# Kernel tuning notes

Hardware: AMD Instinct MI355X
Metric: run time of the kernel (lower is better)

Reference implementation:

```python
import jax, jax.numpy as jnp
import numpy as np

TAU = 0.07
COS_EPS = 1e-8   # torch F.cosine_similarity eps
L1_EPS = 1e-12   # torch F.normalize eps
MM_EPS = 1e-8    # min-max renorm eps

B, C, H, W = 64, 256, 32, 32
S, D = 512, 256


def setup_inputs() -> dict:
    key = jax.random.key(0)
    k1, k2, k3, k4 = jax.random.split(key, 4)
    scale = 1.0 / np.sqrt(D)
    return {
        "image_patches": jax.random.normal(k1, (B, C, H, W), dtype=jnp.float32),
        "text_tokens": jax.random.normal(k2, (B, S, D), dtype=jnp.float32),
        "Wv": jax.random.normal(k3, (D, D), dtype=jnp.float32) * scale,
        "bv": jnp.zeros((D,), dtype=jnp.float32),
        "Wt": jax.random.normal(k4, (D, D), dtype=jnp.float32) * scale,
        "bt": jnp.zeros((D,), dtype=jnp.float32),
    }


def _linear(x, Wgt, b):
    return x @ Wgt.T + b


def _l2n(x, axis=-1):
    n = jnp.maximum(jnp.linalg.norm(x, axis=axis, keepdims=True), COS_EPS)
    return x / n


def _sym_ce_diag(sim):
    # sim [..., N, N]; mean of -log_softmax diagonals along both class axes
    lsm_r = jax.nn.log_softmax(sim, axis=-1)
    lsm_c = jax.nn.log_softmax(sim, axis=-2)
    d_r = jnp.diagonal(lsm_r, axis1=-2, axis2=-1)
    d_c = jnp.diagonal(lsm_c, axis1=-2, axis2=-1)
    return 0.5 * (-jnp.mean(d_r) - jnp.mean(d_c))


def reference(image_patches, text_tokens, Wv, bv, Wt, bt):
    b, c, h, w = image_patches.shape
    hw = h * w
    # b c h w -> b (h w) c, then adapters
    patches = image_patches.reshape(b, c, hw).transpose(0, 2, 1)  # [b, hw, c]
    patches = _linear(patches, Wv, bv)          # [b, hw, d]
    tokens = _linear(text_tokens, Wt, bt)       # [b, s, d]

    # global embeddings: mean-pool then adapter (adapter applied twice on vision path)
    g_img = _linear(jnp.mean(patches, axis=1), Wv, bv)  # [b, d]
    g_txt = _linear(jnp.mean(tokens, axis=1), Wt, bt)   # [b, d]

    # global contrastive loss (cosine sim / tau, symmetric CE over batch)
    g_sim = (_l2n(g_img) @ _l2n(g_txt).T) / TAU         # [b, b]
    global_loss = _sym_ce_diag(g_sim)

    # fine-grained alignment
    sim = jnp.einsum('bpd,bsd->bps', patches, tokens)   # [b, hw, s]
    mn = jnp.min(sim, axis=1, keepdims=True)
    mx = jnp.max(sim, axis=1, keepdims=True)
    sim = (sim - mn) / (mx - mn + MM_EPS)
    sigma = 1.0 / hw
    sim = jnp.where(sim < sigma, 0.0, sim)
    # L1 normalize over patch dim (torch F.normalize p=1 dim=1)
    weights = sim / jnp.maximum(jnp.sum(jnp.abs(sim), axis=1, keepdims=True), L1_EPS)
    lgve = jnp.einsum('bps,bpd->bsd', weights, patches)  # [b, s, d]

    # fine-grained contrastive loss: cosine sim between grouped-vision and text tokens
    f_sim = jnp.einsum('bid,bjd->bij', _l2n(lgve), _l2n(tokens)) / TAU  # [b, s, s]
    fine_loss = _sym_ce_diag(f_sim)

    return global_loss + fine_loss
```

## Files before the change

### kernel.cpp

```cpp
#include <hip/hip_runtime.h>
#include <math.h>

#define BB   64
#define HWP  1024
#define SS   512
#define DD   256
#define TAU_INV (1.0f/0.07f)
#define SIGMA   (1.0f/1024.0f)

typedef unsigned short us;
typedef __attribute__((ext_vector_type(8))) short short8v;
typedef __attribute__((ext_vector_type(8))) unsigned short ushort8v;
typedef __attribute__((ext_vector_type(4))) float floatx4;

__device__ __forceinline__ float bf2f(us u) {
    return __uint_as_float((unsigned)u << 16);
}
__device__ __forceinline__ us f2bf(float f) {
    unsigned u = __float_as_uint(f);
    u += 0x7FFFu + ((u >> 16) & 1u);
    return (us)(u >> 16);
}
__device__ __forceinline__ void split_bf(float v, us& h, us& l) {
    h = f2bf(v);
    l = f2bf(v - bf2f(h));
}

__global__ void zero_out_k(float* out) { if (threadIdx.x == 0) out[0] = 0.0f; }

enum { OPM_F32_ROW = 0, OPM_F32_COL = 1, OPM_SPL_ROW = 2, OPM_SPL_COL = 3,
       OPM_B16_COL = 4, OPM_B16_ROW = 5, OPM_WGT_COL = 6 };
enum { OUT_F32 = 0, OUT_B16 = 1 };

#define LDSTRIDE 40

template<int MODE, int ROWS, int NW>
struct SRegs {
    static constexpr int RR = ROWS / 128;
    static constexpr bool ISF32 = (MODE == OPM_F32_ROW) || (MODE == OPM_F32_COL);
    ushort8v h[ISF32 ? 1 : RR][2];
    ushort8v l[(MODE == OPM_SPL_ROW) ? RR : 1][2];
    float4   f[ISF32 ? RR : 1][4];
};

template<int MODE, int ROWS, int NW>
__device__ __forceinline__ void stage_load(
    const char* p0, const char* p1, int ld, int row0, int k0, int tid,
    SRegs<MODE, ROWS, NW>& R)
{
    #pragma unroll
    for (int rr = 0; rr < ROWS / 128; ++rr) {
        if constexpr (MODE == OPM_SPL_ROW) {
            const us* ph = (const us*)p0;
            const us* pl = (const us*)p1;
            const int i = rr * 128 + (tid >> 1), ko = (tid & 1) * 16;
            const long long g = (long long)(row0 + i) * ld + k0 + ko;
            R.h[rr][0] = *(const ushort8v*)&ph[g];
            R.h[rr][1] = *(const ushort8v*)&ph[g + 8];
            R.l[rr][0] = *(const ushort8v*)&pl[g];
            R.l[rr][1] = *(const ushort8v*)&pl[g + 8];
        } else if constexpr (MODE == OPM_B16_ROW) {
            const us* ph = (const us*)p0;
            if constexpr (NW == 4) {
                const int i = rr * 128 + (tid >> 1), ko = (tid & 1) * 16;
                const long long g = (long long)(row0 + i) * ld + k0 + ko;
                R.h[rr][0] = *(const ushort8v*)&ph[g];
                R.h[rr][1] = *(const ushort8v*)&ph[g + 8];
            } else {
                const int i = rr * 128 + (tid >> 2), ko = (tid & 3) * 8;
                const long long g = (long long)(row0 + i) * ld + k0 + ko;
                R.h[rr][0] = *(const ushort8v*)&ph[g];
            }
        } else if constexpr (MODE == OPM_F32_ROW) {
            const float* pf = (const float*)p0;
            const int i = rr * 128 + (tid >> 1), ko = (tid & 1) * 16;
            const long long g = (long long)(row0 + i) * ld + k0 + ko;
            #pragma unroll
            for (int c = 0; c < 4; ++c)
                R.f[rr][c] = *(const float4*)&pf[g + c * 4];
        } else if constexpr (MODE == OPM_F32_COL) {
            const float* pf = (const float*)p0;
            const int m = rr * 128 + (tid & 127), kh = (tid >> 7) * 16;
            const long long base = (long long)(k0 + kh) * ld + row0 + m;
            #pragma unroll
            for (int c = 0; c < 4; ++c) {
                float4 v;
                v.x = pf[base + (long long)(c * 4 + 0) * ld];
                v.y = pf[base + (long long)(c * 4 + 1) * ld];
                v.z = pf[base + (long long)(c * 4 + 2) * ld];
                v.w = pf[base + (long long)(c * 4 + 3) * ld];
                R.f[rr][c] = v;
            }
        } else {
            const us* ph = (const us*)p0;
            if constexpr (NW == 4) {
                const int m = rr * 128 + (tid & 127), kh = (tid >> 7) * 16;
                const long long base = (long long)(k0 + kh) * ld + row0 + m;
                #pragma unroll
                for (int kk = 0; kk < 8; ++kk) {
                    R.h[rr][0][kk] = ph[base + (long long)kk * ld];
                    R.h[rr][1][kk] = ph[base + (long long)(kk + 8) * ld];
                }
            } else {
                const int m = rr * 128 + (tid & 127), kh = (tid >> 7) * 8;
                const long long base = (long long)(k0 + kh) * ld + row0 + m;
                #pragma unroll
                for (int kk = 0; kk < 8; ++kk)
                    R.h[rr][0][kk] = ph[base + (long long)kk * ld];
            }
        }
    }
}

template<int MODE, int ROWS, int NW>
__device__ __forceinline__ void stage_store(
    const SRegs<MODE, ROWS, NW>& R, us* ldsH, us* ldsL, int tid, float nlo, float inv)
{
    #pragma unroll
    for (int rr = 0; rr < ROWS / 128; ++rr) {
        if constexpr (MODE == OPM_SPL_ROW) {
            const int i = rr * 128 + (tid >> 1), ko = (tid & 1) * 16;
            *(ushort8v*)&ldsH[i * LDSTRIDE + ko]     = R.h[rr][0];
            *(ushort8v*)&ldsH[i * LDSTRIDE + ko + 8] = R.h[rr][1];
            *(ushort8v*)&ldsL[i * LDSTRIDE + ko]     = R.l[rr][0];
            *(ushort8v*)&ldsL[i * LDSTRIDE + ko + 8] = R.l[rr][1];
        } else if constexpr (MODE == OPM_B16_ROW) {
            if constexpr (NW == 4) {
                const int i = rr * 128 + (tid >> 1), ko = (tid & 1) * 16;
                *(ushort8v*)&ldsH[i * LDSTRIDE + ko]     = R.h[rr][0];
                *(ushort8v*)&ldsH[i * LDSTRIDE + ko + 8] = R.h[rr][1];
            } else {
                const int i = rr * 128 + (tid >> 2), ko = (tid & 3) * 8;
                *(ushort8v*)&ldsH[i * LDSTRIDE + ko] = R.h[rr][0];
            }
        } else if constexpr (MODE == OPM_F32_ROW) {
            const int i = rr * 128 + (tid >> 1), ko = (tid & 1) * 16;
            us h16[16], l16a[16];
            #pragma unroll
            for (int c = 0; c < 4; ++c) {
                float4 v = R.f[rr][c];
                split_bf(v.x, h16[c*4+0], l16a[c*4+0]);
                split_bf(v.y, h16[c*4+1], l16a[c*4+1]);
                split_bf(v.z, h16[c*4+2], l16a[c*4+2]);
                split_bf(v.w, h16[c*4+3], l16a[c*4+3]);
            }
            *(ushort8v*)&ldsH[i * LDSTRIDE + ko]     = *(const ushort8v*)&h16[0];
            *(ushort8v*)&ldsH[i * LDSTRIDE + ko + 8] = *(const ushort8v*)&h16[8];
            *(ushort8v*)&ldsL[i * LDSTRIDE + ko]     = *(const ushort8v*)&l16a[0];
            *(ushort8v*)&ldsL[i * LDSTRIDE + ko + 8] = *(const ushort8v*)&l16a[8];
        } else if constexpr (MODE == OPM_F32_COL) {
            const int m = rr * 128 + (tid & 127), kh = (tid >> 7) * 16;
            us vh[16], vl[16];
            #pragma unroll
            for (int c = 0; c < 4; ++c) {
                float4 v = R.f[rr][c];
                split_bf(v.x, vh[c*4+0], vl[c*4+0]);
                split_bf(v.y, vh[c*4+1], vl[c*4+1]);
                split_bf(v.z, vh[c*4+2], vl[c*4+2]);
                split_bf(v.w, vh[c*4+3], vl[c*4+3]);
            }
            *(ushort8v*)&ldsH[m * LDSTRIDE + kh]     = *(const ushort8v*)&vh[0];
            *(ushort8v*)&ldsH[m * LDSTRIDE + kh + 8] = *(const ushort8v*)&vh[8];
            *(ushort8v*)&ldsL[m * LDSTRIDE + kh]     = *(const ushort8v*)&vl[0];
            *(ushort8v*)&ldsL[m * LDSTRIDE + kh + 8] = *(const ushort8v*)&vl[8];
        } else if constexpr (MODE == OPM_B16_COL) {
            if constexpr (NW == 4) {
                const int m = rr * 128 + (tid & 127), kh = (tid >> 7) * 16;
                *(ushort8v*)&ldsH[m * LDSTRIDE + kh]     = R.h[rr][0];
                *(ushort8v*)&ldsH[m * LDSTRIDE + kh + 8] = R.h[rr][1];
            } else {
                const int m = rr * 128 + (tid & 127), kh = (tid >> 7) * 8;
                *(ushort8v*)&ldsH[m * LDSTRIDE + kh] = R.h[rr][0];
            }
        } else if constexpr (MODE == OPM_WGT_COL) {
            if constexpr (NW == 4) {
                const int m = rr * 128 + (tid & 127), kh = (tid >> 7) * 16;
                us v[16];
                #pragma unroll
                for (int kk = 0; kk < 8; ++kk) {
                    const float w0 = fmaf(bf2f(R.h[rr][0][kk]), inv, nlo);
                    const float w1 = fmaf(bf2f(R.h[rr][1][kk]), inv, nlo);
                    v[kk]     = (w0 < SIGMA) ? (us)0 : f2bf(w0);
                    v[kk + 8] = (w1 < SIGMA) ? (us)0 : f2bf(w1);
                }
                *(ushort8v*)&ldsH[m * LDSTRIDE + kh]     = *(const ushort8v*)&v[0];
                *(ushort8v*)&ldsH[m * LDSTRIDE + kh + 8] = *(const ushort8v*)&v[8];
            } else {
                const int m = rr * 128 + (tid & 127), kh = (tid >> 7) * 8;
                us v[8];
                #pragma unroll
                for (int kk = 0; kk < 8; ++kk) {
                    const float w0 = fmaf(bf2f(R.h[rr][0][kk]), inv, nlo);
                    v[kk] = (w0 < SIGMA) ? (us)0 : f2bf(w0);
                }
                *(ushort8v*)&ldsH[m * LDSTRIDE + kh] = *(const ushort8v*)&v[0];
            }
        }
    }
}

template<int AMODE, int BMODE, int OMODE, int EPI, int NT, int PREF, int NW>
__global__ __launch_bounds__(NW * 64) void mfma_gemm(
    const void* A0, const void* A1, const void* B0, const void* B1, void* C0,
    int M, int N, int K, int lda, int ldb, int ldc,
    long long sA, long long sB, long long sC,
    const float* __restrict__ bias, const float* __restrict__ invm,
    const float* __restrict__ invn, float scale,
    const float* __restrict__ wlo, const float* __restrict__ whi,
    float* __restrict__ aux0, float* __restrict__ aux1,
    float* __restrict__ aux2, float* __restrict__ aux3, float* __restrict__ aux4)
{
    constexpr bool ASPL = (AMODE <= OPM_SPL_COL);
    constexpr bool BSPL = (BMODE <= OPM_SPL_COL);
    constexpr int NF = NT / 16;
    constexpr int MI = 8 / NW;
    constexpr int RPW = 128 / NW;
    __shared__ __align__(16) us Ah[128 * LDSTRIDE];
    __shared__ __align__(16) us Al[ASPL ? 128 * LDSTRIDE : 8];
    __shared__ __align__(16) us Bh[NT * LDSTRIDE];
    __shared__ __align__(16) us Bl[BSPL ? NT * LDSTRIDE : 8];
    __shared__ float redm[(EPI >= 3) ? NW * NT : 1];
    __shared__ float reds[(EPI >= 3) ? NW * NT : 1];

    const int tid = threadIdx.x;
    const int w = tid >> 6, lane = tid & 63;
    const int quad = lane >> 4, l16 = lane & 15;

    int bx = blockIdx.x, by = blockIdx.y, bz = blockIdx.z;
    {
        const int nbx = gridDim.x, nby = gridDim.y, nbz = gridDim.z;
        const int nwg = nbx * nby * nbz;
        if ((nwg & 7) == 0) {
            const int hw = bx + nbx * (by + nby * bz);
            const int cpx = nwg >> 3;
            int wk = (hw & 7) * cpx + (hw >> 3);
            bx = wk % nbx; wk /= nbx;
            by = wk % nby; bz = wk / nby;
        }
    }

    const int m0 = bx * 128, n0 = by * NT;
    const int b = bz;

    const char* Ab0 = (const char*)A0 + (long long)b * sA;
    const char* Ab1 = A1 ? (const char*)A1 + (long long)b * sA : nullptr;
    const char* Bb0 = (const char*)B0 + (long long)b * sB;
    const char* Bb1 = B1 ? (const char*)B1 + (long long)b * sB : nullptr;

    float nloA = 0.f, invA = 0.f;
    if constexpr (AMODE == OPM_WGT_COL) {
        const float* wloA = wlo + (long long)b * M;
        const float* whiA = whi + (long long)b * M;
        const float lo = wloA[m0 + (tid & 127)];
        invA = 1.0f / (whiA[m0 + (tid & 127)] - lo + 1e-8f);
        nloA = -lo * invA;
    }

    SRegs<AMODE, 128, NW> RA;
    SRegs<BMODE, NT, NW>  RB;
    if constexpr (PREF) {
        stage_load<AMODE, 128, NW>(Ab0, Ab1, lda, m0, 0, tid, RA);
        stage_load<BMODE, NT, NW>(Bb0, Bb1, ldb, n0, 0, tid, RB);
    }

    floatx4 acc[MI][NF];
    #pragma unroll
    for (int mi = 0; mi < MI; ++mi)
        #pragma unroll
        for (int ni = 0; ni < NF; ++ni)
            acc[mi][ni] = (floatx4){0.f, 0.f, 0.f, 0.f};

    for (int k0 = 0; k0 < K; k0 += 32) {
        if constexpr (!PREF) {
            stage_load<AMODE, 128, NW>(Ab0, Ab1, lda, m0, k0, tid, RA);
            stage_load<BMODE, NT, NW>(Bb0, Bb1, ldb, n0, k0, tid, RB);
        }
        stage_store<AMODE, 128, NW>(RA, Ah, Al, tid, nloA, invA);
        stage_store<BMODE, NT, NW>(RB, Bh, Bl, tid, 0.f, 0.f);
        __syncthreads();

        if constexpr (PREF) {
            if (k0 + 32 < K) {
                stage_load<AMODE, 128, NW>(Ab0, Ab1, lda, m0, k0 + 32, tid, RA);
                stage_load<BMODE, NT, NW>(Bb0, Bb1, ldb, n0, k0 + 32, tid, RB);
            }
        }

        short8v ah[MI], al[MI];
        #pragma unroll
        for (int mi = 0; mi < MI; ++mi) {
            const int r = (RPW * w + 16 * mi + l16) * LDSTRIDE + quad * 8;
            ah[mi] = *(const short8v*)&Ah[r];
            if constexpr (ASPL) al[mi] = *(const short8v*)&Al[r];
        }
        #pragma unroll
        for (int ni = 0; ni < NF; ++ni) {
            const int rB = (16 * ni + l16) * LDSTRIDE + quad * 8;
            short8v bh = *(const short8v*)&Bh[rB];
            #pragma unroll
            for (int mi = 0; mi < MI; ++mi)
                acc[mi][ni] = __builtin_amdgcn_mfma_f32_16x16x32_bf16(ah[mi], bh, acc[mi][ni], 0, 0, 0);
            if constexpr (BSPL) {
                short8v bl = *(const short8v*)&Bl[rB];
                #pragma unroll
                for (int mi = 0; mi < MI; ++mi)
                    acc[mi][ni] = __builtin_amdgcn_mfma_f32_16x16x32_bf16(ah[mi], bl, acc[mi][ni], 0, 0, 0);
            }
            if constexpr (ASPL) {
                #pragma unroll
                for (int mi = 0; mi < MI; ++mi)
                    acc[mi][ni] = __builtin_amdgcn_mfma_f32_16x16x32_bf16(al[mi], bh, acc[mi][ni], 0, 0, 0);
            }
        }
        __syncthreads();
    }

    if constexpr (EPI != 4) {
        char* Cb0 = (char*)C0 + (long long)b * sC;
        #pragma unroll
        for (int mi = 0; mi < MI; ++mi)
            #pragma unroll
            for (int ni = 0; ni < NF; ++ni)
                #pragma unroll
                for (int r = 0; r < 4; ++r) {
                    const int row = m0 + RPW * w + 16 * mi + quad * 4 + r;
                    const int col = n0 + 16 * ni + l16;
                    float v = acc[mi][ni][r];
                    if constexpr (EPI == 1) v += bias[col];
                    const long long idx = (long long)row * ldc + col;
                    if constexpr (OMODE == OUT_F32) ((float*)Cb0)[idx] = v;
                    else                            ((us*)Cb0)[idx] = f2bf(v);
                }
    }

    if constexpr (EPI == 3) {
        #pragma unroll
        for (int ni = 0; ni < NF; ++ni) {
            float lo = 1e30f, hi = -1e30f;
            #pragma unroll
            for (int mi = 0; mi < MI; ++mi)
                #pragma unroll
                for (int r = 0; r < 4; ++r) {
                    const float vr = bf2f(f2bf(acc[mi][ni][r]));
                    lo = fminf(lo, vr); hi = fmaxf(hi, vr);
                }
            lo = fminf(lo, __shfl_xor(lo, 16)); lo = fminf(lo, __shfl_xor(lo, 32));
            hi = fmaxf(hi, __shfl_xor(hi, 16)); hi = fmaxf(hi, __shfl_xor(hi, 32));
            if (quad == 0) {
                redm[w * NT + 16 * ni + l16] = lo;
                reds[w * NT + 16 * ni + l16] = hi;
            }
        }
        __syncthreads();
        if (tid < NT) {
            float lo = 1e30f, hi = -1e30f;
            #pragma unroll
            for (int w4 = 0; w4 < NW; ++w4) {
                lo = fminf(lo, redm[w4 * NT + tid]);
                hi = fmaxf(hi, reds[w4 * NT + tid]);
            }
            const long long o = ((long long)b * N + n0 + tid) * 8 + bx;
            aux0[o] = lo; aux1[o] = hi;
        }
    }

    if constexpr (EPI == 4) {
        float bn[NF];
        #pragma unroll
        for (int ni = 0; ni < NF; ++ni)
            bn[ni] = invn[(long long)b * N + n0 + 16 * ni + l16] * scale;
        float amv[MI * 4];
        #pragma unroll
        for (int mi = 0; mi < MI; ++mi)
            #pragma unroll
            for (int r = 0; r < 4; ++r)
                amv[mi * 4 + r] = invm[(long long)b * M + m0 + RPW * w + 16 * mi + quad * 4 + r];

        #pragma unroll
        for (int mi = 0; mi < MI; ++mi)
            #pragma unroll
            for (int r = 0; r < 4; ++r) {
                const int grow = m0 + RPW * w + 16 * mi + quad * 4 + r;
                float vv[NF];
                float rm = -1e30f;
                #pragma unroll
                for (int ni = 0; ni < NF; ++ni) {
                    const float v = acc[mi][ni][r] * amv[mi * 4 + r] * bn[ni];
                    vv[ni] = v;
                    rm = fmaxf(rm, v);
                    if (grow == n0 + 16 * ni + l16)
                        aux4[(long long)b * M + grow] = v;
                }
                #pragma unroll
                for (int o = 8; o > 0; o >>= 1) rm = fmaxf(rm, __shfl_xor(rm, o));
                float rs = 0.f;
                #pragma unroll
                for (int ni = 0; ni < NF; ++ni) rs += expf(vv[ni] - rm);
                #pragma unroll
                for (int o = 8; o > 0; o >>= 1) rs += __shfl_xor(rs, o);
                if (l16 == 0) {
                    const long long o = ((long long)b * M + grow) * 4 + by;
                    aux0[o] = rm; aux1[o] = rs;
                }
            }

        #pragma unroll
        for (int ni = 0; ni < NF; ++ni) {
            float va[MI * 4];
            float cm = -1e30f;
            #pragma unroll
            for (int mi = 0; mi < MI; ++mi)
                #pragma unroll
                for (int r = 0; r < 4; ++r) {
                    const float v = acc[mi][ni][r] * amv[mi * 4 + r] * bn[ni];
                    va[mi * 4 + r] = v;
                    cm = fmaxf(cm, v);
                }
            cm = fmaxf(cm, __shfl_xor(cm, 16));
            cm = fmaxf(cm, __shfl_xor(cm, 32));
            float cs = 0.f;
            #pragma unroll
            for (int j = 0; j < MI * 4; ++j) cs += expf(va[j] - cm);
            cs += __shfl_xor(cs, 16);
            cs += __shfl_xor(cs, 32);
            if (quad == 0) {
                redm[w * NT + 16 * ni + l16] = cm;
                reds[w * NT + 16 * ni + l16] = cs;
            }
        }
        __syncthreads();
        if (tid < NT) {
            float m = -1e30f, s = 0.f;
            #pragma unroll
            for (int w4 = 0; w4 < NW; ++w4) {
                const float cm = redm[w4 * NT + tid], cs = reds[w4 * NT + tid];
                const float nm = fmaxf(m, cm);
                s = s * expf(m - nm) + cs * expf(cm - nm);
                m = nm;
            }
            const long long o = ((long long)b * N + n0 + tid) * 4 + bx;
            aux2[o] = m; aux3[o] = s;
        }
    }
}


__global__ __launch_bounds__(256) void convert_w_k(
    const float* Wv, const float* Wt, us* Wvh, us* Wvl, us* Wth, us* Wtl)
{
    const int i = blockIdx.x * 256 + threadIdx.x;
    split_bf(Wv[i], Wvh[i], Wvl[i]);
    split_bf(Wt[i], Wth[i], Wtl[i]);
}

__global__ __launch_bounds__(256) void mean_img_k(
    const float* __restrict__ img, float* __restrict__ mimg)
{
    const int row = blockIdx.x * 4 + (threadIdx.x >> 6);
    const int lane = threadIdx.x & 63;
    const float* p = img + (long long)row * 1024;
    float s = 0.f;
    #pragma unroll
    for (int c = 0; c < 4; ++c) {
        float4 v = *(const float4*)&p[(c * 64 + lane) * 4];
        s += v.x + v.y + v.z + v.w;
    }
    #pragma unroll
    for (int o = 32; o > 0; o >>= 1) s += __shfl_xor(s, o);
    if (lane == 0) mimg[row] = s * (1.0f / 1024.0f);
}

__global__ __launch_bounds__(256) void mean_text_s1(
    const float* __restrict__ text, float* __restrict__ part)
{
    const int b = blockIdx.x, ch = blockIdx.y, k = threadIdx.x;
    const float* p = text + ((long long)b * 512 + ch * 64) * 256 + k;
    float s = 0.f;
    for (int r = 0; r < 64; ++r) s += p[r * 256];
    part[(b * 8 + ch) * 256 + k] = s;
}
__global__ __launch_bounds__(256) void mean_text_s2(
    const float* __restrict__ part, float* __restrict__ mt)
{
    const int b = blockIdx.x, k = threadIdx.x;
    float s = 0.f;
    for (int c = 0; c < 8; ++c) s += part[(b * 8 + c) * 256 + k];
    mt[b * 256 + k] = s * (1.0f / 512.0f);
}

__global__ __launch_bounds__(256) void small_adapter_k(
    const float* __restrict__ x, const float* __restrict__ W,
    const float* __restrict__ bias, float* __restrict__ y)
{
    const int b = blockIdx.x, d = threadIdx.x;
    __shared__ float xs[256];
    xs[d] = x[b * 256 + d];
    __syncthreads();
    const float4* w = (const float4*)(W + (long long)d * 256);
    const float4* xv = (const float4*)xs;
    float s = bias[d];
    #pragma unroll 8
    for (int k = 0; k < 64; ++k) {
        const float4 a = xv[k], ww = w[k];
        s += a.x * ww.x + a.y * ww.y + a.z * ww.z + a.w * ww.w;
    }
    y[b * 256 + d] = s;
}


__global__ __launch_bounds__(256) void inv_norm_f32_k(
    const float* __restrict__ x, float* __restrict__ inv)
{
    const int row = blockIdx.x * 4 + (threadIdx.x >> 6);
    const int lane = threadIdx.x & 63;
    float4 v = *(const float4*)&x[(long long)row * 256 + lane * 4];
    float s = v.x * v.x + v.y * v.y + v.z * v.z + v.w * v.w;
    #pragma unroll
    for (int o = 32; o > 0; o >>= 1) s += __shfl_xor(s, o);
    if (lane == 0) inv[row] = 1.0f / fmaxf(sqrtf(s), 1e-8f);
}

__global__ __launch_bounds__(256) void g_sim_k(
    const float* __restrict__ gi, const float* __restrict__ gt,
    const float* __restrict__ invI, const float* __restrict__ invT,
    float* __restrict__ gs)
{
    const int i = blockIdx.x, t = threadIdx.x;
    const int j = t >> 2, part = t & 3;
    __shared__ float a[256];
    a[t] = gi[i * 256 + t];
    __syncthreads();
    const float* bp = gt + (long long)j * 256 + part * 64;
    const float* ap = a + part * 64;
    float s = 0.f;
    #pragma unroll 16
    for (int k = 0; k < 64; ++k) s += ap[k] * bp[k];
    s += __shfl_xor(s, 1);
    s += __shfl_xor(s, 2);
    if (part == 0) gs[i * 64 + j] = s * invI[i] * invT[j] * TAU_INV;
}

__global__ __launch_bounds__(64) void g_lse_k(
    const float* __restrict__ gs, float* __restrict__ out)
{
    const int b = blockIdx.x, lane = threadIdx.x;
    const bool is_col = b >= 64;
    const int r = is_col ? b - 64 : b;
    const float v = is_col ? gs[lane * 64 + r] : gs[r * 64 + lane];
    float m = v;
    #pragma unroll
    for (int o = 32; o > 0; o >>= 1) m = fmaxf(m, __shfl_xor(m, o));
    float s = expf(v - m);
    #pragma unroll
    for (int o = 32; o > 0; o >>= 1) s += __shfl_xor(s, o);
    if (lane == 0)
        atomicAdd(out, ((m + logf(s)) - gs[r * 64 + r]) * (0.5f / 64.0f));
}

__global__ __launch_bounds__(256) void inv_norm_b16_k(
    const us* __restrict__ x, float* __restrict__ inv)
{
    const int row = blockIdx.x * 4 + (threadIdx.x >> 6);
    const int lane = threadIdx.x & 63;
    ushort4 h = *(const ushort4*)&x[(long long)row * 256 + lane * 4];
    const float x0 = bf2f(h.x), x1 = bf2f(h.y), x2 = bf2f(h.z), x3 = bf2f(h.w);
    float s = x0 * x0 + x1 * x1 + x2 * x2 + x3 * x3;
    #pragma unroll
    for (int o = 32; o > 0; o >>= 1) s += __shfl_xor(s, o);
    if (lane == 0) inv[row] = 1.0f / fmaxf(sqrtf(s), 1e-8f);
}


__global__ __launch_bounds__(256) void minmax_merge_k(
    const float* __restrict__ mnp, const float* __restrict__ mxp,
    float* __restrict__ mn, float* __restrict__ mx)
{
    const int idx = blockIdx.x * 256 + threadIdx.x;
    float lo = 1e30f, hi = -1e30f;
    #pragma unroll
    for (int c = 0; c < 8; ++c) {
        lo = fminf(lo, mnp[(long long)idx * 8 + c]);
        hi = fmaxf(hi, mxp[(long long)idx * 8 + c]);
    }
    mn[idx] = lo; mx[idx] = hi;
}

__global__ __launch_bounds__(256) void fine_merge4_k(
    const float* __restrict__ pm, const float* __restrict__ ps,
    const float* __restrict__ diag, float* __restrict__ out)
{
    const int idx = blockIdx.x * 256 + threadIdx.x;
    float m = -1e30f, s = 0.f;
    #pragma unroll
    for (int c = 0; c < 4; ++c) {
        const float cm = pm[(long long)idx * 4 + c], cs = ps[(long long)idx * 4 + c];
        const float nm = fmaxf(m, cm);
        s = s * expf(m - nm) + cs * expf(cm - nm);
        m = nm;
    }
    const float contrib = (m + logf(s)) - diag[idx];
    __shared__ float red[256];
    red[threadIdx.x] = contrib;
    __syncthreads();
    for (int w = 128; w > 0; w >>= 1) {
        if (threadIdx.x < w) red[threadIdx.x] += red[threadIdx.x + w];
        __syncthreads();
    }
    if (threadIdx.x == 0) atomicAdd(out, red[0] * (0.5f / (64.0f * 512.0f)));
}

extern "C" void kernel_launch(void* const* d_in, const int* in_sizes, int n_in,
                              void* d_out, int out_size, void* d_ws, size_t ws_size,
                              hipStream_t stream)
{
    const float* img  = (const float*)d_in[0];
    const float* text = (const float*)d_in[1];
    const float* Wv   = (const float*)d_in[2];
    const float* bv   = (const float*)d_in[3];
    const float* Wt   = (const float*)d_in[4];
    const float* bt   = (const float*)d_in[5];
    float* out = (float*)d_out;
    char* ws = (char*)d_ws;

    us* patches = (us*)(ws + 0);
    us* tokens  = (us*)(ws + 33554432);
    us* simW    = (us*)(ws + 50331648);
    us* lgve    = (us*)(ws + 117440512);
    char* st = ws + 134217728;
    float* mean_img  = (float*)(st + 0);
    float* mean_text = (float*)(st + 65536);
    float* mean_pat  = (float*)(st + 131072);
    float* mean_tok  = (float*)(st + 196608);
    float* g_img     = (float*)(st + 262144);
    float* g_txt     = (float*)(st + 327680);
    float* textpart  = (float*)(st + 393216);
    float* mnp       = (float*)(st + 917504);
    float* mxp       = (float*)(st + 1966080);
    float* mnv       = (float*)(st + 3014656);
    float* mxv       = (float*)(st + 3145728);
    float* inv_l     = (float*)(st + 3276800);
    float* inv_t     = (float*)(st + 3407872);
    us* Wvh = (us*)(st + 3538944);
    us* Wvl = (us*)(st + 3670016);
    us* Wth = (us*)(st + 3801088);
    us* Wtl = (us*)(st + 3932160);
    float* inv_gi  = (float*)(st + 4063232);
    float* inv_gt  = (float*)(st + 4063744);
    float* g_simbf = (float*)(st + 4064256);
    float* pm_row  = (float*)(st + 4194304);
    float* ps_row  = (float*)(st + 4718592);
    float* pm_col  = (float*)(st + 5242880);
    float* ps_col  = (float*)(st + 5767168);
    float* diag    = (float*)(st + 6291456);

    zero_out_k<<<1, 64, 0, stream>>>(out);
    convert_w_k<<<256, 256, 0, stream>>>(Wv, Wt, Wvh, Wvl, Wth, Wtl);

    mean_img_k<<<4096, 256, 0, stream>>>(img, mean_img);
    mean_text_s1<<<dim3(64, 8), 256, 0, stream>>>(text, textpart);
    mean_text_s2<<<64, 256, 0, stream>>>(textpart, mean_text);
    small_adapter_k<<<BB, 256, 0, stream>>>(mean_img, Wv, bv, mean_pat);
    small_adapter_k<<<BB, 256, 0, stream>>>(mean_pat, Wv, bv, g_img);
    small_adapter_k<<<BB, 256, 0, stream>>>(mean_text, Wt, bt, mean_tok);
    small_adapter_k<<<BB, 256, 0, stream>>>(mean_tok, Wt, bt, g_txt);
    inv_norm_f32_k<<<16, 256, 0, stream>>>(g_img, inv_gi);
    inv_norm_f32_k<<<16, 256, 0, stream>>>(g_txt, inv_gt);
    g_sim_k<<<64, 256, 0, stream>>>(g_img, g_txt, inv_gi, inv_gt, g_simbf);
    g_lse_k<<<128, 64, 0, stream>>>(g_simbf, out);

    mfma_gemm<OPM_F32_COL, OPM_SPL_ROW, OUT_B16, 1, 256, 0, 4><<<dim3(8, 1, BB), 256, 0, stream>>>(
        img, nullptr, Wvh, Wvl, patches,
        1024, 256, 256, 1024, 256, 256,
        1048576LL, 0LL, 524288LL, bv, nullptr, nullptr, 0.f, nullptr, nullptr,
        nullptr, nullptr, nullptr, nullptr, nullptr);

    mfma_gemm<OPM_F32_ROW, OPM_SPL_ROW, OUT_B16, 1, 256, 0, 4><<<dim3(4, 1, BB), 256, 0, stream>>>(
        text, nullptr, Wth, Wtl, tokens,
        512, 256, 256, 256, 256, 256,
        524288LL, 0LL, 262144LL, bt, nullptr, nullptr, 0.f, nullptr, nullptr,
        nullptr, nullptr, nullptr, nullptr, nullptr);

    mfma_gemm<OPM_B16_ROW, OPM_B16_ROW, OUT_B16, 3, 128, 1, 4><<<dim3(8, 4, BB), 256, 0, stream>>>(
        patches, nullptr, tokens, nullptr, simW,
        1024, 512, 256, 256, 256, 512,
        524288LL, 262144LL, 1048576LL, nullptr, nullptr, nullptr, 0.f, nullptr, nullptr,
        mnp, mxp, nullptr, nullptr, nullptr);

    minmax_merge_k<<<128, 256, 0, stream>>>(mnp, mxp, mnv, mxv);

    mfma_gemm<OPM_WGT_COL, OPM_B16_COL, OUT_B16, 0, 128, 1, 8><<<dim3(4, 2, BB), 512, 0, stream>>>(
        simW, nullptr, patches, nullptr, lgve,
        512, 256, 1024, 512, 256, 256,
        1048576LL, 524288LL, 262144LL, nullptr, nullptr, nullptr, 0.f, mnv, mxv,
        nullptr, nullptr, nullptr, nullptr, nullptr);

    inv_norm_b16_k<<<8192, 256, 0, stream>>>(lgve, inv_l);
    inv_norm_b16_k<<<8192, 256, 0, stream>>>(tokens, inv_t);

    mfma_gemm<OPM_B16_ROW, OPM_B16_ROW, OUT_B16, 4, 128, 1, 8><<<dim3(4, 4, BB), 512, 0, stream>>>(
        lgve, nullptr, tokens, nullptr, nullptr,
        512, 512, 256, 256, 256, 512,
        262144LL, 262144LL, 0LL, nullptr, inv_l, inv_t, TAU_INV, nullptr, nullptr,
        pm_row, ps_row, pm_col, ps_col, diag);

    fine_merge4_k<<<128, 256, 0, stream>>>(pm_row, ps_row, diag, out);
    fine_merge4_k<<<128, 256, 0, stream>>>(pm_col, ps_col, diag, out);
}
```

Baseline: 397.8 us.

## Deepen GEMM global prefetch to two register stages with lighter barriers

```diff
diff --git a/kernel.cpp b/kernel.cpp
--- a/kernel.cpp
+++ b/kernel.cpp
@@ -256,11 +256,13 @@
         nloA = -lo * invA;
     }
 
-    SRegs<AMODE, 128, NW> RA;
-    SRegs<BMODE, NT, NW>  RB;
+    SRegs<AMODE, 128, NW> RA0, RA1;
+    SRegs<BMODE, NT, NW>  RB0, RB1;
     if constexpr (PREF) {
-        stage_load<AMODE, 128, NW>(Ab0, Ab1, lda, m0, 0, tid, RA);
-        stage_load<BMODE, NT, NW>(Bb0, Bb1, ldb, n0, 0, tid, RB);
+        stage_load<AMODE, 128, NW>(Ab0, Ab1, lda, m0, 0, tid, RA0);
+        stage_load<BMODE, NT, NW>(Bb0, Bb1, ldb, n0, 0, tid, RB0);
+        stage_load<AMODE, 128, NW>(Ab0, Ab1, lda, m0, 32, tid, RA1);
+        stage_load<BMODE, NT, NW>(Bb0, Bb1, ldb, n0, 32, tid, RB1);
     }
 
     floatx4 acc[MI][NF];
@@ -270,22 +272,7 @@
         for (int ni = 0; ni < NF; ++ni)
             acc[mi][ni] = (floatx4){0.f, 0.f, 0.f, 0.f};
 
-    for (int k0 = 0; k0 < K; k0 += 32) {
-        if constexpr (!PREF) {
-            stage_load<AMODE, 128, NW>(Ab0, Ab1, lda, m0, k0, tid, RA);
-            stage_load<BMODE, NT, NW>(Bb0, Bb1, ldb, n0, k0, tid, RB);
-        }
-        stage_store<AMODE, 128, NW>(RA, Ah, Al, tid, nloA, invA);
-        stage_store<BMODE, NT, NW>(RB, Bh, Bl, tid, 0.f, 0.f);
-        __syncthreads();
-
-        if constexpr (PREF) {
-            if (k0 + 32 < K) {
-                stage_load<AMODE, 128, NW>(Ab0, Ab1, lda, m0, k0 + 32, tid, RA);
-                stage_load<BMODE, NT, NW>(Bb0, Bb1, ldb, n0, k0 + 32, tid, RB);
-            }
-        }
-
+    auto do_mfma = [&]() {
         short8v ah[MI], al[MI];
         #pragma unroll
         for (int mi = 0; mi < MI; ++mi) {
@@ -312,8 +299,40 @@
                     acc[mi][ni] = __builtin_amdgcn_mfma_f32_16x16x32_bf16(al[mi], bh, acc[mi][ni], 0, 0, 0);
             }
         }
-        __syncthreads();
-    }
+    };
+
+#define GEMM_SUBSTEP(RAx, RBx, KCUR, KNEXT)                                    \
+    do {                                                                       \
+        if constexpr (!PREF) {                                                 \
+            stage_load<AMODE, 128, NW>(Ab0, Ab1, lda, m0, (KCUR), tid, RAx);   \
+            stage_load<BMODE, NT, NW>(Bb0, Bb1, ldb, n0, (KCUR), tid, RBx);    \
+        }                                                                      \
+        stage_store<AMODE, 128, NW>(RAx, Ah, Al, tid, nloA, invA);             \
+        stage_store<BMODE, NT, NW>(RBx, Bh, Bl, tid, 0.f, 0.f);                \
+        if constexpr (PREF) {                                                  \
+            asm volatile("s_waitcnt lgkmcnt(0)" ::: "memory");                 \
+            __builtin_amdgcn_s_barrier();                                      \
+            if ((KNEXT) < K) {                                                 \
+                stage_load<AMODE, 128, NW>(Ab0, Ab1, lda, m0, (KNEXT), tid, RAx); \
+                stage_load<BMODE, NT, NW>(Bb0, Bb1, ldb, n0, (KNEXT), tid, RBx);  \
+            }                                                                  \
+        } else {                                                               \
+            __syncthreads();                                                   \
+        }                                                                      \
+        do_mfma();                                                             \
+        if constexpr (PREF) {                                                  \
+            asm volatile("s_waitcnt lgkmcnt(0)" ::: "memory");                 \
+            __builtin_amdgcn_s_barrier();                                      \
+        } else {                                                               \
+            __syncthreads();                                                   \
+        }                                                                      \
+    } while (0)
+
+    for (int k0 = 0; k0 < K; k0 += 64) {
+        GEMM_SUBSTEP(RA0, RB0, k0, k0 + 64);
+        GEMM_SUBSTEP(RA1, RB1, k0 + 32, k0 + 96);
+    }
+#undef GEMM_SUBSTEP
 
     if constexpr (EPI != 4) {
         char* Cb0 = (char*)C0 + (long long)b * sC;
```

After: 388.3 us. 2.4% less time.
